# Kernel optimization log

Hardware: AMD Instinct MI355X
Metric: run time of the kernel (lower is better)

## Reference

```python
import jax, jax.numpy as jnp
import numpy as np

N_NODES = 100000
N_EDGES = 1600000
N_DATE = 5000  # last N_DATE nodes are date nodes [0,0,1]
D_IN = 128
D_H = 128
N_CLASSES = 16
MLP_HID = 8


def setup_inputs() -> dict:
    key = jax.random.key(0)
    ks = jax.random.split(key, 12)
    feature = jax.random.normal(ks[0], (N_NODES, D_IN), dtype=jnp.float32)
    edge_weight = jax.random.uniform(ks[1], (N_EDGES,), dtype=jnp.float32)
    src = jax.random.randint(ks[2], (N_EDGES,), 0, N_NODES, dtype=jnp.int32)
    dst = jax.random.randint(ks[3], (N_EDGES,), 0, N_NODES, dtype=jnp.int32)
    # node_type one-hot: regular nodes [1,0,0], last N_DATE nodes are date nodes [0,0,1]
    nt = np.zeros((N_NODES, 3), dtype=np.int32)
    nt[: N_NODES - N_DATE, 0] = 1
    nt[N_NODES - N_DATE :, 2] = 1
    node_type = jnp.asarray(nt)
    # GraphConv weights (xavier uniform) + zero bias, DGL convention: h @ W, W:[in,out]
    def xavier(k, fan_in, fan_out):
        lim = float(np.sqrt(6.0 / (fan_in + fan_out)))
        return jax.random.uniform(k, (fan_in, fan_out), jnp.float32, -lim, lim)
    W0 = xavier(ks[4], D_IN, D_H)
    b0 = jnp.zeros((D_H,), jnp.float32)
    W1 = xavier(ks[5], D_H, D_H)
    b1 = jnp.zeros((D_H,), jnp.float32)
    mlp_w1 = xavier(ks[6], D_H, MLP_HID)
    mlp_b1 = jnp.zeros((MLP_HID,), jnp.float32)
    mlp_w2 = xavier(ks[7], MLP_HID, N_CLASSES)
    mlp_b2 = jnp.zeros((N_CLASSES,), jnp.float32)
    return {
        "feature": feature, "edge_weight": edge_weight, "src": src, "dst": dst,
        "node_type": node_type, "W0": W0, "b0": b0, "W1": W1, "b1": b1,
        "mlp_w1": mlp_w1, "mlp_b1": mlp_b1, "mlp_w2": mlp_w2, "mlp_b2": mlp_b2,
    }


def reference(feature, edge_weight, src, dst, node_type,
              W0, b0, W1, b1, mlp_w1, mlp_b1, mlp_w2, mlp_b2):
    n = feature.shape[0]
    ones_e = jnp.ones_like(edge_weight)
    # unweighted degrees (DGL norm='both'), clamped to >= 1
    deg_out = jnp.clip(jax.ops.segment_sum(ones_e, src, num_segments=n), 1.0)
    deg_in = jnp.clip(jax.ops.segment_sum(ones_e, dst, num_segments=n), 1.0)
    norm_src = deg_out ** -0.5  # [N]
    norm_dst = deg_in ** -0.5   # [N]

    def graph_conv(h, W, b):
        hn = h * norm_src[:, None]                      # D_out^{-1/2} src scaling
        msg = hn[src] * edge_weight[:, None]            # [E, d] edge-weighted gather
        agg = jax.ops.segment_sum(msg, dst, num_segments=n)  # scatter-add
        return (agg * norm_dst[:, None]) @ W + b        # D_in^{-1/2}, then linear

    h = jax.nn.relu(graph_conv(feature, W0, b0))
    h = jax.nn.relu(graph_conv(h, W1, b1))

    # sum-pool over date nodes ([0,0,1]) == tail slice in original layout
    date_mask = ((node_type[:, 0] == 0) & (node_type[:, 1] == 0) & (node_type[:, 2] == 1)).astype(h.dtype)
    cnt = date_mask.sum()
    pooled = (h * date_mask[:, None]).sum(axis=0) / cnt  # [d_h]

    hid = jax.nn.relu(pooled @ mlp_w1 + mlp_b1)
    return hid @ mlp_w2 + mlp_b2  # [num_classes]
```

## Files before the change

kernel.cpp:

```cpp
#include <hip/hip_runtime.h>
#include <hip/hip_fp16.h>
#include <hip/hip_fp8.h>
#include <stdint.h>

#define D 128
#define GT 16
#define SLOTS 48
#define EPB 4096
#define PTB 1024
#define CAPE 5120
#define MAXB 400
#define MAXDATE 8192
#define WPN 16384
#define PWAVES 8

typedef _Float16 f16x8 __attribute__((ext_vector_type(8)));
typedef float    f32x4 __attribute__((ext_vector_type(4)));
typedef float    f32x2 __attribute__((ext_vector_type(2)));

__global__ __launch_bounds__(PTB) void partition_kernel(
    const int* __restrict__ src, const int* __restrict__ dst, const float* __restrict__ ew,
    int* __restrict__ cursorA, int* __restrict__ cursorB,
    int2* __restrict__ ebuf, unsigned char* __restrict__ sbuf, int E, int nbk) {
    __shared__ int histA[MAXB], histB[MAXB], baseA[MAXB], baseB[MAXB];
    int tid = threadIdx.x;
    for (int i = tid; i < nbk; i += PTB) { histA[i] = 0; histB[i] = 0; }
    __syncthreads();
    int e0 = blockIdx.x * EPB;
    int dcache[EPB / PTB], scache[EPB / PTB];
    float wcache[EPB / PTB];
    #pragma unroll
    for (int i = 0; i < EPB / PTB; ++i) {
        int e = e0 + i * PTB + tid;
        bool ok = e < E;
        dcache[i] = ok ? dst[e] : -1;
        scache[i] = ok ? src[e] : 0;
        wcache[i] = ok ? ew[e] : 0.f;
        if (ok) {
            atomicAdd(&histA[dcache[i] >> 8], 1);
            atomicAdd(&histB[scache[i] >> 8], 1);
        }
    }
    __syncthreads();
    for (int i = tid; i < nbk; i += PTB) {
        baseA[i] = atomicAdd(&cursorA[i], histA[i]);
        baseB[i] = atomicAdd(&cursorB[i], histB[i]);
        histA[i] = 0; histB[i] = 0;
    }
    __syncthreads();
    #pragma unroll
    for (int i = 0; i < EPB / PTB; ++i) {
        if (dcache[i] >= 0) {
            int d = dcache[i], s = scache[i];
            int bA = d >> 8;
            int pA = baseA[bA] + atomicAdd(&histA[bA], 1);
            if (pA < CAPE) ebuf[(size_t)bA * CAPE + pA] =
                make_int2(s | ((d & 255) << 17), __float_as_int(wcache[i]));
            int bB = s >> 8;
            int pB = baseB[bB] + atomicAdd(&histB[bB], 1);
            if (pB < CAPE) sbuf[(size_t)bB * CAPE + pB] = (unsigned char)(s & 255);
        }
    }
}

__global__ __launch_bounds__(256) void build_count_kernel(
    const int2* __restrict__ ebuf, const int* __restrict__ cursorA,
    const unsigned char* __restrict__ sbuf, const int* __restrict__ cursorB,
    int2* __restrict__ ell, int* __restrict__ deg_in, int* __restrict__ deg_out,
    int n, int nbk) {
    __shared__ int lcur[256];
    int tid = threadIdx.x;
    lcur[tid] = 0;
    __syncthreads();
    if (blockIdx.x < (unsigned)nbk) {
        int b = blockIdx.x;
        int cntE = min(cursorA[b], CAPE);
        const int2* buf = ebuf + (size_t)b * CAPE;
        for (int i = tid; i < cntE; i += 256) {
            int2 r = buf[i];
            int s = r.x & 0x1FFFF;
            int dlow = (r.x >> 17) & 255;
            int slot = atomicAdd(&lcur[dlow], 1);
            int node = (b << 8) + dlow;
            if (slot < SLOTS) ell[(size_t)node * SLOTS + slot] = make_int2(s, r.y);
        }
        __syncthreads();
        int v = (b << 8) + tid;
        if (v < n) deg_in[v] = lcur[tid];
    } else {
        int b = blockIdx.x - nbk;
        int cntS = min(cursorB[b], CAPE);
        const unsigned char* buf = sbuf + (size_t)b * CAPE;
        const unsigned int* buf32 = (const unsigned int*)buf;
        int nw = cntS >> 2;
        for (int i = tid; i < nw; i += 256) {
            unsigned int wv = buf32[i];
            atomicAdd(&lcur[wv & 255], 1);
            atomicAdd(&lcur[(wv >> 8) & 255], 1);
            atomicAdd(&lcur[(wv >> 16) & 255], 1);
            atomicAdd(&lcur[wv >> 24], 1);
        }
        if (tid < (cntS & 3)) atomicAdd(&lcur[buf[(nw << 2) + tid]], 1);
        __syncthreads();
        int v = (b << 8) + tid;
        if (v < n) deg_out[v] = lcur[tid];
    }
}

__global__ void norm_flag_kernel(const int* __restrict__ deg_out, const int* __restrict__ deg_in,
                                 const int* __restrict__ node_type,
                                 float* __restrict__ norm_src, float* __restrict__ norm_dst,
                                 int* __restrict__ list, int* __restrict__ cnt,
                                 unsigned char* __restrict__ flag, int n) {
    int v = blockIdx.x * blockDim.x + threadIdx.x;
    if (v < n) {
        float d_o = (float)max(deg_out[v], 1);
        float d_i = (float)max(deg_in[v], 1);
        norm_src[v] = 1.0f / sqrtf(d_o);
        norm_dst[v] = 1.0f / sqrtf(d_i);
        flag[v] = 0;
        int t0 = node_type[v * 3 + 0];
        int t1 = node_type[v * 3 + 1];
        int t2 = node_type[v * 3 + 2];
        if (t0 == 0 && t1 == 0 && t2 == 1) {
            int idx = atomicAdd(cnt, 1);
            list[idx] = v;
        }
    }
}

__global__ __launch_bounds__(256) void mark_kernel(
    const int* __restrict__ list, const int* __restrict__ cnt,
    const int2* __restrict__ ell, const int* __restrict__ deg_in,
    unsigned char* __restrict__ flag) {
    int wave = (blockIdx.x * 256 + threadIdx.x) >> 6;
    int lane = threadIdx.x & 63;
    if (wave >= min(*cnt, MAXDATE)) return;
    int v = __builtin_amdgcn_readfirstlane(list[wave]);
    int m = min(deg_in[v], SLOTS);
    if (lane < m) {
        int s = ell[(size_t)v * SLOTS + lane].x;
        flag[s] = 1;
    }
}

__global__ __launch_bounds__(256) void compact_kernel(
    const unsigned char* __restrict__ flag, const int* __restrict__ deg_in,
    int* __restrict__ list2, int* __restrict__ cnt2, int n) {
    int v = blockIdx.x * 256 + threadIdx.x;
    int lane = threadIdx.x & 63;
    bool f = (v < n) && (flag[v] != 0);
    unsigned long long mask = __ballot(f);
    int base = 0;
    if (lane == 0 && mask) base = atomicAdd(cnt2, __popcll(mask));
    base = __shfl(base, 0);
    if (f) {
        int off = __builtin_amdgcn_mbcnt_hi((unsigned int)(mask >> 32),
                  __builtin_amdgcn_mbcnt_lo((unsigned int)mask, 0));
        list2[base + off] = v | (min(deg_in[v], SLOTS) << 17);
    }
}

__global__ __launch_bounds__(256) void wpack_kernel(const float* __restrict__ W,
                                                    _Float16* __restrict__ wp,
                                                    int* __restrict__ cursorAB,
                                                    float* __restrict__ pooled,
                                                    int* __restrict__ cnt) {
    int tid = threadIdx.x;
    if (blockIdx.x == 0) {
        for (int i = tid; i < 2 * MAXB; i += 256) cursorAB[i] = 0;
        if (tid < D) pooled[tid] = 0.f;
        if (tid == 0) { cnt[0] = 0; cnt[1] = 0; }
    }
    int base = blockIdx.x * 256 + tid;
    for (int idx = base; idx < WPN; idx += gridDim.x * 256) {
        int j = idx & 7;
        int l = (idx >> 3) & 63;
        int c = (idx >> 9) & 7;
        int k0b = idx >> 12;
        int q = l >> 4, r = l & 15;
        float w = W[(k0b * 32 + q * 8 + j) * 128 + c * 16 + r];
        _Float16 hi = (_Float16)w;
        wp[idx] = hi;
        wp[idx + WPN] = (_Float16)(w - (float)hi);
    }
}

__global__ __launch_bounds__(512) void gemm_mfma_kernel(
    const float* __restrict__ X, const float* __restrict__ ns,
    const _Float16* __restrict__ wp, unsigned char* __restrict__ P8, int n) {
    __shared__ _Float16 wl[2 * WPN];
    int tid  = threadIdx.x;
    int lane = tid & 63;
    int wib  = tid >> 6;
    {
        const ulonglong2* src16 = (const ulonglong2*)wp;
        ulonglong2* dst16 = (ulonglong2*)wl;
        #pragma unroll
        for (int i = 0; i < (2 * WPN * 2) / (512 * 16); ++i)
            dst16[i * 512 + tid] = src16[i * 512 + tid];
    }
    __syncthreads();

    int q = lane >> 4, r = lane & 15;
    int row0 = blockIdx.x * 128 + wib * 16;
    if (row0 >= n) return;
    int ra = min(row0 + r, n - 1);
    float sa = ns[ra];

    float4 x[8];
    #pragma unroll
    for (int kb = 0; kb < 4; ++kb) {
        x[2 * kb]     = *(const float4*)&X[(size_t)ra * 128 + kb * 32 + q * 8];
        x[2 * kb + 1] = *(const float4*)&X[(size_t)ra * 128 + kb * 32 + q * 8 + 4];
    }
    f16x8 a[4];
    #pragma unroll
    for (int kb = 0; kb < 4; ++kb) {
        a[kb][0] = (_Float16)(x[2 * kb].x * sa);
        a[kb][1] = (_Float16)(x[2 * kb].y * sa);
        a[kb][2] = (_Float16)(x[2 * kb].z * sa);
        a[kb][3] = (_Float16)(x[2 * kb].w * sa);
        a[kb][4] = (_Float16)(x[2 * kb + 1].x * sa);
        a[kb][5] = (_Float16)(x[2 * kb + 1].y * sa);
        a[kb][6] = (_Float16)(x[2 * kb + 1].z * sa);
        a[kb][7] = (_Float16)(x[2 * kb + 1].w * sa);
    }

    f32x4 acc[8];
    #pragma unroll
    for (int c = 0; c < 8; ++c) acc[c] = (f32x4){0.f, 0.f, 0.f, 0.f};

    const _Float16* wb = wl + lane * 8;
    #pragma unroll
    for (int c = 0; c < 8; ++c) {
        #pragma unroll
        for (int kb = 0; kb < 4; ++kb) {
            f16x8 bh = *(const f16x8*)&wb[kb * 4096 + c * 512];
            f16x8 bl = *(const f16x8*)&wb[kb * 4096 + c * 512 + WPN];
            acc[c] = __builtin_amdgcn_mfma_f32_16x16x32_f16(bh, a[kb], acc[c], 0, 0, 0);
            acc[c] = __builtin_amdgcn_mfma_f32_16x16x32_f16(bl, a[kb], acc[c], 0, 0, 0);
        }
    }

    int row = row0 + r;
    if (row < n) {
        #pragma unroll
        for (int c = 0; c < 8; ++c) {
            int w0 = __builtin_amdgcn_cvt_pk_fp8_f32(acc[c][0], acc[c][1], 0, false);
            int w1 = __builtin_amdgcn_cvt_pk_fp8_f32(acc[c][2], acc[c][3], w0, true);
            *(unsigned int*)&P8[(size_t)row * 128 + c * 16 + q * 4] = (unsigned int)w1;
        }
    }
}

__global__ __launch_bounds__(256) void gather1_kernel(
    const unsigned char* __restrict__ P8, const int2* __restrict__ ell,
    const float* __restrict__ norm_src, const float* __restrict__ norm_dst,
    const float* __restrict__ bias, const int* __restrict__ list2,
    const int* __restrict__ cnt2, __half* __restrict__ h1) {
    int wave = (blockIdx.x * 256 + threadIdx.x) >> 6;
    int lane = threadIdx.x & 63;
    int nn = __builtin_amdgcn_readfirstlane(*cnt2);
    if (wave >= nn) return;
    int pk = __builtin_amdgcn_readfirstlane(list2[wave]);
    int v = pk & 0x1FFFF;
    int m = pk >> 17;
    int half = lane >> 5;
    int l32  = lane & 31;
    const int2* row = ell + (size_t)v * SLOTS;
    const unsigned int* P32 = (const unsigned int*)P8;
    float nd = norm_dst[v];
    float ns = norm_src[v];
    float4 acc = make_float4(0.f, 0.f, 0.f, 0.f);

    if (m <= 16) {
        int4 q[8];
        #pragma unroll
        for (int i = 0; i < 8; ++i) q[i] = *(const int4*)&row[2 * i];
        unsigned int r[8];
        float w[8];
        #pragma unroll
        for (int i = 0; i < 8; ++i) {
            bool ok = (2 * i + half) < m;
            int s = ok ? (half ? q[i].z : q[i].x) : 0;
            w[i] = ok ? __int_as_float(half ? q[i].w : q[i].y) : 0.f;
            r[i] = P32[(size_t)s * 32 + l32];
        }
        #pragma unroll
        for (int i = 0; i < 8; ++i) {
            f32x2 c0 = __builtin_amdgcn_cvt_pk_f32_fp8((int)r[i], false);
            f32x2 c1 = __builtin_amdgcn_cvt_pk_f32_fp8((int)r[i], true);
            acc.x = fmaf(w[i], c0[0], acc.x);
            acc.y = fmaf(w[i], c0[1], acc.y);
            acc.z = fmaf(w[i], c1[0], acc.z);
            acc.w = fmaf(w[i], c1[1], acc.w);
        }
    } else {
        int4 q[16];
        #pragma unroll
        for (int i = 0; i < 16; ++i) q[i] = *(const int4*)&row[2 * i];
        unsigned int r[16];
        float w[16];
        #pragma unroll
        for (int i = 0; i < 16; ++i) {
            bool ok = (2 * i + half) < m;
            int s = ok ? (half ? q[i].z : q[i].x) : 0;
            w[i] = ok ? __int_as_float(half ? q[i].w : q[i].y) : 0.f;
            r[i] = P32[(size_t)s * 32 + l32];
        }
        #pragma unroll
        for (int i = 0; i < 16; ++i) {
            f32x2 c0 = __builtin_amdgcn_cvt_pk_f32_fp8((int)r[i], false);
            f32x2 c1 = __builtin_amdgcn_cvt_pk_f32_fp8((int)r[i], true);
            acc.x = fmaf(w[i], c0[0], acc.x);
            acc.y = fmaf(w[i], c0[1], acc.y);
            acc.z = fmaf(w[i], c1[0], acc.z);
            acc.w = fmaf(w[i], c1[1], acc.w);
        }
        if (m > 32) {
            for (int e = 32; e < m; e += 4) {
                int4 qa = *(const int4*)&row[e];
                int4 qb = *(const int4*)&row[e + 2];
                int2 p0 = half ? make_int2(qa.z, qa.w) : make_int2(qa.x, qa.y);
                int2 p1 = half ? make_int2(qb.z, qb.w) : make_int2(qb.x, qb.y);
                bool v0 = (e + half) < m;
                bool v1 = (e + 2 + half) < m;
                int s0 = v0 ? p0.x : 0;
                int s1 = v1 ? p1.x : 0;
                unsigned int r0 = P32[(size_t)s0 * 32 + l32];
                unsigned int r1 = P32[(size_t)s1 * 32 + l32];
                float w0 = v0 ? __int_as_float(p0.y) : 0.f;
                float w1 = v1 ? __int_as_float(p1.y) : 0.f;
                f32x2 c0 = __builtin_amdgcn_cvt_pk_f32_fp8((int)r0, false);
                f32x2 c1 = __builtin_amdgcn_cvt_pk_f32_fp8((int)r0, true);
                f32x2 d0 = __builtin_amdgcn_cvt_pk_f32_fp8((int)r1, false);
                f32x2 d1 = __builtin_amdgcn_cvt_pk_f32_fp8((int)r1, true);
                acc.x = fmaf(w0, c0[0], acc.x); acc.x = fmaf(w1, d0[0], acc.x);
                acc.y = fmaf(w0, c0[1], acc.y); acc.y = fmaf(w1, d0[1], acc.y);
                acc.z = fmaf(w0, c1[0], acc.z); acc.z = fmaf(w1, d1[0], acc.z);
                acc.w = fmaf(w0, c1[1], acc.w); acc.w = fmaf(w1, d1[1], acc.w);
            }
        }
    }

    acc.x += __shfl_xor(acc.x, 32);
    acc.y += __shfl_xor(acc.y, 32);
    acc.z += __shfl_xor(acc.z, 32);
    acc.w += __shfl_xor(acc.w, 32);
    if (half == 0) {
        float4 b4 = ((const float4*)bias)[l32];
        float ra = fmaxf(fmaf(acc.x, nd, b4.x), 0.f) * ns;
        float rb = fmaxf(fmaf(acc.y, nd, b4.y), 0.f) * ns;
        float rc = fmaxf(fmaf(acc.z, nd, b4.z), 0.f) * ns;
        float rd = fmaxf(fmaf(acc.w, nd, b4.w), 0.f) * ns;
        __half2 h0 = __floats2half2_rn(ra, rb);
        __half2 h1v = __floats2half2_rn(rc, rd);
        uint2 u;
        u.x = *(unsigned int*)&h0;
        u.y = *(unsigned int*)&h1v;
        ((uint2*)h1)[(size_t)v * 32 + l32] = u;
    }
}

__global__ __launch_bounds__(256) void gather2_list_kernel(
    const __half* __restrict__ h, const int* __restrict__ deg_in,
    const int2* __restrict__ ell, const float* __restrict__ norm_dst,
    const int* __restrict__ list, const int* __restrict__ cnt,
    float* __restrict__ out) {
    int wave = (blockIdx.x * 256 + threadIdx.x) >> 6;
    int lane = threadIdx.x & 63;
    if (wave >= min(*cnt, MAXDATE)) return;
    int v = __builtin_amdgcn_readfirstlane(list[wave]);
    int half = lane >> 5;
    int l32  = lane & 31;
    const int2* row = ell + (size_t)v * SLOTS;
    int dg = deg_in[v];
    int4 q[16];
    #pragma unroll
    for (int i = 0; i < 16; ++i) q[i] = *(const int4*)&row[2 * i];
    int m = min(dg, SLOTS);
    float2 r[16];
    float w[16];
    #pragma unroll
    for (int i = 0; i < 16; ++i) {
        bool ok = (2 * i + half) < m;
        int s = ok ? (half ? q[i].z : q[i].x) : 0;
        w[i] = ok ? __int_as_float(half ? q[i].w : q[i].y) : 0.f;
        r[i] = ((const float2*)h)[(size_t)s * 32 + l32];
    }
    float4 acc = make_float4(0.f, 0.f, 0.f, 0.f);
    #pragma unroll
    for (int i = 0; i < 16; ++i) {
        float2 a01 = __half22float2(*(const __half2*)&r[i].x);
        float2 a23 = __half22float2(*(const __half2*)&r[i].y);
        acc.x = fmaf(w[i], a01.x, acc.x);
        acc.y = fmaf(w[i], a01.y, acc.y);
        acc.z = fmaf(w[i], a23.x, acc.z);
        acc.w = fmaf(w[i], a23.y, acc.w);
    }
    if (m > 32) {
        for (int e = 32; e < m; e += 4) {
            int4 qa = *(const int4*)&row[e];
            int4 qb = *(const int4*)&row[e + 2];
            int2 p0 = half ? make_int2(qa.z, qa.w) : make_int2(qa.x, qa.y);
            int2 p1 = half ? make_int2(qb.z, qb.w) : make_int2(qb.x, qb.y);
            bool v0 = (e + half) < m;
            bool v1 = (e + 2 + half) < m;
            int s0 = v0 ? p0.x : 0;
            int s1 = v1 ? p1.x : 0;
            float2 raw0 = ((const float2*)h)[(size_t)s0 * 32 + l32];
            float2 raw1 = ((const float2*)h)[(size_t)s1 * 32 + l32];
            float w0 = v0 ? __int_as_float(p0.y) : 0.f;
            float w1 = v1 ? __int_as_float(p1.y) : 0.f;
            float2 a01 = __half22float2(*(const __half2*)&raw0.x);
            float2 a23 = __half22float2(*(const __half2*)&raw0.y);
            float2 b01 = __half22float2(*(const __half2*)&raw1.x);
            float2 b23 = __half22float2(*(const __half2*)&raw1.y);
            acc.x = fmaf(w0, a01.x, acc.x); acc.x = fmaf(w1, b01.x, acc.x);
            acc.y = fmaf(w0, a01.y, acc.y); acc.y = fmaf(w1, b01.y, acc.y);
            acc.z = fmaf(w0, a23.x, acc.z); acc.z = fmaf(w1, b23.x, acc.z);
            acc.w = fmaf(w0, a23.y, acc.w); acc.w = fmaf(w1, b23.y, acc.w);
        }
    }
    acc.x += __shfl_xor(acc.x, 32);
    acc.y += __shfl_xor(acc.y, 32);
    acc.z += __shfl_xor(acc.z, 32);
    acc.w += __shfl_xor(acc.w, 32);
    if (half == 0) {
        float nd = norm_dst[v];
        ((float4*)(out + (size_t)wave * D))[l32] =
            make_float4(acc.x * nd, acc.y * nd, acc.z * nd, acc.w * nd);
    }
}

__global__ __launch_bounds__(512) void gemm_pool_kernel(
    const float* __restrict__ X, const float* __restrict__ W,
    const float* __restrict__ bias, const int* __restrict__ cnt,
    float* __restrict__ pooled) {
    __shared__ float wlds[D * D];
    __shared__ float rows[PWAVES][GT * D];
    int tid  = threadIdx.x;
    int lane = tid & 63;
    int wib  = tid >> 6;

    const float4* W4 = (const float4*)W;
    for (int i = tid; i < (D * D) / 4; i += 512)
        *(float4*)&wlds[i * 4] = W4[i];
    __syncthreads();

    int m = min(*cnt, MAXDATE);
    int ntiles = (m + GT - 1) / GT;
    float2 bb = ((const float2*)bias)[lane];
    float psx = 0.f, psy = 0.f;
    bool any = false;
    float* rw = rows[wib];
    const float2* X2 = (const float2*)X;

    for (int tile = blockIdx.x * PWAVES + wib; tile < ntiles; tile += gridDim.x * PWAVES) {
        int t0 = tile * GT;
        any = true;
        #pragma unroll
        for (int t = 0; t < GT; ++t) {
            int i = t0 + t;
            float2 r = (i < m) ? X2[(size_t)i * 64 + lane] : make_float2(0.f, 0.f);
            *(float2*)&rw[t * D + 2 * lane] = r;
        }
        __builtin_amdgcn_wave_barrier();

        float2 acc[GT];
        #pragma unroll
        for (int t = 0; t < GT; ++t) acc[t] = make_float2(0.f, 0.f);

        for (int k = 0; k < D; k += 4) {
            float2 w0 = *(const float2*)&wlds[(k + 0) * D + 2 * lane];
            float2 w1 = *(const float2*)&wlds[(k + 1) * D + 2 * lane];
            float2 w2 = *(const float2*)&wlds[(k + 2) * D + 2 * lane];
            float2 w3 = *(const float2*)&wlds[(k + 3) * D + 2 * lane];
            #pragma unroll
            for (int t = 0; t < GT; ++t) {
                float4 r = *(const float4*)&rw[t * D + k];
                acc[t].x = fmaf(r.x, w0.x, acc[t].x); acc[t].y = fmaf(r.x, w0.y, acc[t].y);
                acc[t].x = fmaf(r.y, w1.x, acc[t].x); acc[t].y = fmaf(r.y, w1.y, acc[t].y);
                acc[t].x = fmaf(r.z, w2.x, acc[t].x); acc[t].y = fmaf(r.z, w2.y, acc[t].y);
                acc[t].x = fmaf(r.w, w3.x, acc[t].x); acc[t].y = fmaf(r.w, w3.y, acc[t].y);
            }
        }

        #pragma unroll
        for (int t = 0; t < GT; ++t) {
            if (t0 + t < m) {
                psx += fmaxf(acc[t].x + bb.x, 0.f);
                psy += fmaxf(acc[t].y + bb.y, 0.f);
            }
        }
        __builtin_amdgcn_wave_barrier();
    }

    if (any) {
        atomicAdd(&pooled[2 * lane + 0], psx);
        atomicAdd(&pooled[2 * lane + 1], psy);
    }
}

__global__ void mlp_kernel(const float* __restrict__ pooled, const int* __restrict__ cnt,
                           const float* __restrict__ w1, const float* __restrict__ b1,
                           const float* __restrict__ w2, const float* __restrict__ b2,
                           float* __restrict__ out) {
    __shared__ float hid[8];
    int t = threadIdx.x;
    float inv = 1.0f / (float)(*cnt);
    if (t < 8) {
        float a = b1[t];
        for (int k = 0; k < 128; ++k) a = fmaf(pooled[k] * inv, w1[k * 8 + t], a);
        hid[t] = fmaxf(a, 0.f);
    }
    __syncthreads();
    if (t < 16) {
        float a = b2[t];
        for (int j = 0; j < 8; ++j) a = fmaf(hid[j], w2[j * 16 + t], a);
        out[t] = a;
    }
}

extern "C" void kernel_launch(void* const* d_in, const int* in_sizes, int n_in,
                              void* d_out, int out_size, void* d_ws, size_t ws_size,
                              hipStream_t stream) {
    const float* feature   = (const float*)d_in[0];
    const float* ew        = (const float*)d_in[1];
    const int*   src       = (const int*)d_in[2];
    const int*   dst       = (const int*)d_in[3];
    const int*   node_type = (const int*)d_in[4];
    const float* W0        = (const float*)d_in[5];
    const float* b0        = (const float*)d_in[6];
    const float* W1        = (const float*)d_in[7];
    const float* b1        = (const float*)d_in[8];
    const float* mw1       = (const float*)d_in[9];
    const float* mb1       = (const float*)d_in[10];
    const float* mw2       = (const float*)d_in[11];
    const float* mb2       = (const float*)d_in[12];
    float* out = (float*)d_out;

    const int n = in_sizes[0] / D;
    const int E = in_sizes[1];
    const int NBK = (n + 255) >> 8;

    char* ws = (char*)d_ws;
    size_t off = 0;
    auto alloc = [&](size_t bytes) -> void* {
        void* p = ws + off;
        off = (off + bytes + 255) & ~(size_t)255;
        return p;
    };
    int*           cursorAB = (int*)alloc(2 * MAXB * 4);
    int*           deg_in   = (int*)alloc((size_t)n * 4);
    int*           deg_out  = (int*)alloc((size_t)n * 4);
    float*         norm_src = (float*)alloc((size_t)n * 4);
    float*         norm_dst = (float*)alloc((size_t)n * 4);
    int*           list     = (int*)alloc((size_t)n * 4);
    int*           list2    = (int*)alloc((size_t)n * 4);
    unsigned char* flag     = (unsigned char*)alloc((size_t)n);
    int2*          ell      = (int2*)alloc(((size_t)n * SLOTS + 8) * 8);
    int2*          ebuf     = (int2*)alloc((size_t)NBK * CAPE * 8);
    unsigned char* sbuf     = (unsigned char*)alloc((size_t)NBK * CAPE);
    unsigned char* P8       = (unsigned char*)alloc((size_t)n * D);
    __half*        h1       = (__half*)alloc((size_t)n * D * 2);
    _Float16*      wp       = (_Float16*)alloc(2 * WPN * 2);
    float*         pooled   = (float*)alloc(D * 4);
    int*           cnt      = (int*)alloc(256);
    float*         agg      = (float*)ebuf;

    int* cursorA = cursorAB;
    int* cursorB = cursorAB + MAXB;
    int* cnt2    = cnt + 1;

    const int TB = 256;
    int pblk = (E + EPB - 1) / EPB;
    int nblk = (n + TB - 1) / TB;

    wpack_kernel<<<16, TB, 0, stream>>>(W0, wp, cursorAB, pooled, cnt);
    partition_kernel<<<pblk, PTB, 0, stream>>>(src, dst, ew, cursorA, cursorB, ebuf, sbuf, E, NBK);
    build_count_kernel<<<2 * NBK, TB, 0, stream>>>(ebuf, cursorA, sbuf, cursorB,
                                                   ell, deg_in, deg_out, n, NBK);
    norm_flag_kernel<<<nblk, TB, 0, stream>>>(deg_out, deg_in, node_type,
                                              norm_src, norm_dst, list, cnt, flag, n);
    mark_kernel<<<(MAXDATE * 64) / TB, TB, 0, stream>>>(list, cnt, ell, deg_in, flag);
    compact_kernel<<<nblk, TB, 0, stream>>>(flag, deg_in, list2, cnt2, n);

    gemm_mfma_kernel<<<(n + 127) / 128, 512, 0, stream>>>(feature, norm_src, wp, P8, n);

    gather1_kernel<<<(n * 64 + TB - 1) / TB, TB, 0, stream>>>(
        P8, ell, norm_src, norm_dst, b0, list2, cnt2, h1);

    gather2_list_kernel<<<(MAXDATE * 64) / TB, TB, 0, stream>>>(
        h1, deg_in, ell, norm_dst, list, cnt, agg);
    gemm_pool_kernel<<<64, 512, 0, stream>>>(agg, W1, b1, cnt, pooled);

    mlp_kernel<<<1, 64, 0, stream>>>(pooled, cnt, mw1, mb1, mw2, mb2, out);
}
```

Before: 273.3 us.

## Mark date-node sources during partition and fuse norm, flag and compaction kernels

The date-node mask now becomes a bitmap in the weight-pack kernel, which also clears the flag array. The partition kernel marks the source of every edge pointing into a date node directly, so the separate mark kernel that read the ELL rows is gone. Norm computation, date-list building and source compaction are fused into one kernel, cutting two launches and an extra pass over node arrays. The layer-2 gather also gains a short path for nodes with at most 16 in-edges, so fewer unused slot loads are issued. One behaviour change: marking from raw edges counts all in-edges, not only the first SLOTS kept in ELL.

```diff
diff --git a/kernel.cpp b/kernel.cpp
--- a/kernel.cpp
+++ b/kernel.cpp
@@ -18,10 +18,54 @@
 typedef float    f32x4 __attribute__((ext_vector_type(4)));
 typedef float    f32x2 __attribute__((ext_vector_type(2)));
 
+__global__ __launch_bounds__(256) void wpack_kernel(const float* __restrict__ W,
+                                                    _Float16* __restrict__ wp,
+                                                    int* __restrict__ cursorAB,
+                                                    float* __restrict__ pooled,
+                                                    int* __restrict__ cnt,
+                                                    const int* __restrict__ node_type,
+                                                    unsigned int* __restrict__ bitmap,
+                                                    int* __restrict__ flag32, int n) {
+    int tid = threadIdx.x;
+    int gt  = blockIdx.x * 256 + tid;
+    int gsz = gridDim.x * 256;
+    int lane = tid & 63;
+    if (blockIdx.x == 0) {
+        for (int i = tid; i < 2 * MAXB; i += 256) cursorAB[i] = 0;
+        if (tid < D) pooled[tid] = 0.f;
+        if (tid == 0) { cnt[0] = 0; cnt[1] = 0; }
+    }
+    int nround = (n + 63) & ~63;
+    for (int v = gt; v < nround; v += gsz) {
+        bool isd = false;
+        if (v < n) {
+            isd = (node_type[v * 3 + 0] == 0) && (node_type[v * 3 + 1] == 0) &&
+                  (node_type[v * 3 + 2] == 1);
+        }
+        unsigned long long msk = __ballot(isd);
+        if (lane == 0)  bitmap[v >> 5] = (unsigned int)msk;
+        if (lane == 32) bitmap[v >> 5] = (unsigned int)(msk >> 32);
+    }
+    for (int i = gt; i < ((n + 3) >> 2); i += gsz) flag32[i] = 0;
+    for (int idx = gt; idx < WPN; idx += gsz) {
+        int j = idx & 7;
+        int l = (idx >> 3) & 63;
+        int c = (idx >> 9) & 7;
+        int k0b = idx >> 12;
+        int q = l >> 4, r = l & 15;
+        float w = W[(k0b * 32 + q * 8 + j) * 128 + c * 16 + r];
+        _Float16 hi = (_Float16)w;
+        wp[idx] = hi;
+        wp[idx + WPN] = (_Float16)(w - (float)hi);
+    }
+}
+
 __global__ __launch_bounds__(PTB) void partition_kernel(
     const int* __restrict__ src, const int* __restrict__ dst, const float* __restrict__ ew,
     int* __restrict__ cursorA, int* __restrict__ cursorB,
-    int2* __restrict__ ebuf, unsigned char* __restrict__ sbuf, int E, int nbk) {
+    int2* __restrict__ ebuf, unsigned char* __restrict__ sbuf,
+    const unsigned int* __restrict__ bitmap, unsigned char* __restrict__ flag,
+    int E, int nbk) {
     __shared__ int histA[MAXB], histB[MAXB], baseA[MAXB], baseB[MAXB];
     int tid = threadIdx.x;
     for (int i = tid; i < nbk; i += PTB) { histA[i] = 0; histB[i] = 0; }
@@ -29,6 +73,7 @@
     int e0 = blockIdx.x * EPB;
     int dcache[EPB / PTB], scache[EPB / PTB];
     float wcache[EPB / PTB];
+    unsigned int dmask = 0;
     #pragma unroll
     for (int i = 0; i < EPB / PTB; ++i) {
         int e = e0 + i * PTB + tid;
@@ -39,6 +84,7 @@
         if (ok) {
             atomicAdd(&histA[dcache[i] >> 8], 1);
             atomicAdd(&histB[scache[i] >> 8], 1);
+            if ((bitmap[dcache[i] >> 5] >> (dcache[i] & 31)) & 1) dmask |= 1u << i;
         }
     }
     __syncthreads();
@@ -59,6 +105,7 @@
             int bB = s >> 8;
             int pB = baseB[bB] + atomicAdd(&histB[bB], 1);
             if (pB < CAPE) sbuf[(size_t)bB * CAPE + pB] = (unsigned char)(s & 255);
+            if ((dmask >> i) & 1) flag[s] = 1;
         }
     }
 }
@@ -107,49 +154,27 @@
     }
 }
 
-__global__ void norm_flag_kernel(const int* __restrict__ deg_out, const int* __restrict__ deg_in,
-                                 const int* __restrict__ node_type,
-                                 float* __restrict__ norm_src, float* __restrict__ norm_dst,
-                                 int* __restrict__ list, int* __restrict__ cnt,
-                                 unsigned char* __restrict__ flag, int n) {
-    int v = blockIdx.x * blockDim.x + threadIdx.x;
-    if (v < n) {
-        float d_o = (float)max(deg_out[v], 1);
-        float d_i = (float)max(deg_in[v], 1);
-        norm_src[v] = 1.0f / sqrtf(d_o);
-        norm_dst[v] = 1.0f / sqrtf(d_i);
-        flag[v] = 0;
-        int t0 = node_type[v * 3 + 0];
-        int t1 = node_type[v * 3 + 1];
-        int t2 = node_type[v * 3 + 2];
-        if (t0 == 0 && t1 == 0 && t2 == 1) {
-            int idx = atomicAdd(cnt, 1);
-            list[idx] = v;
-        }
-    }
-}
-
-__global__ __launch_bounds__(256) void mark_kernel(
-    const int* __restrict__ list, const int* __restrict__ cnt,
-    const int2* __restrict__ ell, const int* __restrict__ deg_in,
-    unsigned char* __restrict__ flag) {
-    int wave = (blockIdx.x * 256 + threadIdx.x) >> 6;
-    int lane = threadIdx.x & 63;
-    if (wave >= min(*cnt, MAXDATE)) return;
-    int v = __builtin_amdgcn_readfirstlane(list[wave]);
-    int m = min(deg_in[v], SLOTS);
-    if (lane < m) {
-        int s = ell[(size_t)v * SLOTS + lane].x;
-        flag[s] = 1;
-    }
-}
-
-__global__ __launch_bounds__(256) void compact_kernel(
-    const unsigned char* __restrict__ flag, const int* __restrict__ deg_in,
+__global__ __launch_bounds__(256) void norm_compact_kernel(
+    const int* __restrict__ deg_out, const int* __restrict__ deg_in,
+    const unsigned int* __restrict__ bitmap, const unsigned char* __restrict__ flag,
+    float* __restrict__ norm_src, float* __restrict__ norm_dst,
+    int* __restrict__ list, int* __restrict__ cnt,
     int* __restrict__ list2, int* __restrict__ cnt2, int n) {
     int v = blockIdx.x * 256 + threadIdx.x;
     int lane = threadIdx.x & 63;
-    bool f = (v < n) && (flag[v] != 0);
+    bool inb = v < n;
+    int di = 0;
+    if (inb) {
+        int d_o = max(deg_out[v], 1);
+        di = deg_in[v];
+        norm_src[v] = 1.0f / sqrtf((float)d_o);
+        norm_dst[v] = 1.0f / sqrtf((float)max(di, 1));
+        if ((bitmap[v >> 5] >> (v & 31)) & 1) {
+            int idx = atomicAdd(cnt, 1);
+            list[idx] = v;
+        }
+    }
+    bool f = inb && (flag[v] != 0);
     unsigned long long mask = __ballot(f);
     int base = 0;
     if (lane == 0 && mask) base = atomicAdd(cnt2, __popcll(mask));
@@ -157,32 +182,7 @@
     if (f) {
         int off = __builtin_amdgcn_mbcnt_hi((unsigned int)(mask >> 32),
                   __builtin_amdgcn_mbcnt_lo((unsigned int)mask, 0));
-        list2[base + off] = v | (min(deg_in[v], SLOTS) << 17);
-    }
-}
-
-__global__ __launch_bounds__(256) void wpack_kernel(const float* __restrict__ W,
-                                                    _Float16* __restrict__ wp,
-                                                    int* __restrict__ cursorAB,
-                                                    float* __restrict__ pooled,
-                                                    int* __restrict__ cnt) {
-    int tid = threadIdx.x;
-    if (blockIdx.x == 0) {
-        for (int i = tid; i < 2 * MAXB; i += 256) cursorAB[i] = 0;
-        if (tid < D) pooled[tid] = 0.f;
-        if (tid == 0) { cnt[0] = 0; cnt[1] = 0; }
-    }
-    int base = blockIdx.x * 256 + tid;
-    for (int idx = base; idx < WPN; idx += gridDim.x * 256) {
-        int j = idx & 7;
-        int l = (idx >> 3) & 63;
-        int c = (idx >> 9) & 7;
-        int k0b = idx >> 12;
-        int q = l >> 4, r = l & 15;
-        float w = W[(k0b * 32 + q * 8 + j) * 128 + c * 16 + r];
-        _Float16 hi = (_Float16)w;
-        wp[idx] = hi;
-        wp[idx + WPN] = (_Float16)(w - (float)hi);
+        list2[base + off] = v | (min(di, SLOTS) << 17);
     }
 }
 
@@ -375,52 +375,76 @@
     int half = lane >> 5;
     int l32  = lane & 31;
     const int2* row = ell + (size_t)v * SLOTS;
-    int dg = deg_in[v];
-    int4 q[16];
-    #pragma unroll
-    for (int i = 0; i < 16; ++i) q[i] = *(const int4*)&row[2 * i];
-    int m = min(dg, SLOTS);
-    float2 r[16];
-    float w[16];
-    #pragma unroll
-    for (int i = 0; i < 16; ++i) {
-        bool ok = (2 * i + half) < m;
-        int s = ok ? (half ? q[i].z : q[i].x) : 0;
-        w[i] = ok ? __int_as_float(half ? q[i].w : q[i].y) : 0.f;
-        r[i] = ((const float2*)h)[(size_t)s * 32 + l32];
-    }
+    int m = min(__builtin_amdgcn_readfirstlane(deg_in[v]), SLOTS);
     float4 acc = make_float4(0.f, 0.f, 0.f, 0.f);
-    #pragma unroll
-    for (int i = 0; i < 16; ++i) {
-        float2 a01 = __half22float2(*(const __half2*)&r[i].x);
-        float2 a23 = __half22float2(*(const __half2*)&r[i].y);
-        acc.x = fmaf(w[i], a01.x, acc.x);
-        acc.y = fmaf(w[i], a01.y, acc.y);
-        acc.z = fmaf(w[i], a23.x, acc.z);
-        acc.w = fmaf(w[i], a23.y, acc.w);
-    }
-    if (m > 32) {
-        for (int e = 32; e < m; e += 4) {
-            int4 qa = *(const int4*)&row[e];
-            int4 qb = *(const int4*)&row[e + 2];
-            int2 p0 = half ? make_int2(qa.z, qa.w) : make_int2(qa.x, qa.y);
-            int2 p1 = half ? make_int2(qb.z, qb.w) : make_int2(qb.x, qb.y);
-            bool v0 = (e + half) < m;
-            bool v1 = (e + 2 + half) < m;
-            int s0 = v0 ? p0.x : 0;
-            int s1 = v1 ? p1.x : 0;
-            float2 raw0 = ((const float2*)h)[(size_t)s0 * 32 + l32];
-            float2 raw1 = ((const float2*)h)[(size_t)s1 * 32 + l32];
-            float w0 = v0 ? __int_as_float(p0.y) : 0.f;
-            float w1 = v1 ? __int_as_float(p1.y) : 0.f;
-            float2 a01 = __half22float2(*(const __half2*)&raw0.x);
-            float2 a23 = __half22float2(*(const __half2*)&raw0.y);
-            float2 b01 = __half22float2(*(const __half2*)&raw1.x);
-            float2 b23 = __half22float2(*(const __half2*)&raw1.y);
-            acc.x = fmaf(w0, a01.x, acc.x); acc.x = fmaf(w1, b01.x, acc.x);
-            acc.y = fmaf(w0, a01.y, acc.y); acc.y = fmaf(w1, b01.y, acc.y);
-            acc.z = fmaf(w0, a23.x, acc.z); acc.z = fmaf(w1, b23.x, acc.z);
-            acc.w = fmaf(w0, a23.y, acc.w); acc.w = fmaf(w1, b23.y, acc.w);
+
+    if (m <= 16) {
+        int4 q[8];
+        #pragma unroll
+        for (int i = 0; i < 8; ++i) q[i] = *(const int4*)&row[2 * i];
+        float2 r[8];
+        float w[8];
+        #pragma unroll
+        for (int i = 0; i < 8; ++i) {
+            bool ok = (2 * i + half) < m;
+            int s = ok ? (half ? q[i].z : q[i].x) : 0;
+            w[i] = ok ? __int_as_float(half ? q[i].w : q[i].y) : 0.f;
+            r[i] = ((const float2*)h)[(size_t)s * 32 + l32];
+        }
+        #pragma unroll
+        for (int i = 0; i < 8; ++i) {
+            float2 a01 = __half22float2(*(const __half2*)&r[i].x);
+            float2 a23 = __half22float2(*(const __half2*)&r[i].y);
+            acc.x = fmaf(w[i], a01.x, acc.x);
+            acc.y = fmaf(w[i], a01.y, acc.y);
+            acc.z = fmaf(w[i], a23.x, acc.z);
+            acc.w = fmaf(w[i], a23.y, acc.w);
+        }
+    } else {
+        int4 q[16];
+        #pragma unroll
+        for (int i = 0; i < 16; ++i) q[i] = *(const int4*)&row[2 * i];
+        float2 r[16];
+        float w[16];
+        #pragma unroll
+        for (int i = 0; i < 16; ++i) {
+            bool ok = (2 * i + half) < m;
+            int s = ok ? (half ? q[i].z : q[i].x) : 0;
+            w[i] = ok ? __int_as_float(half ? q[i].w : q[i].y) : 0.f;
+            r[i] = ((const float2*)h)[(size_t)s * 32 + l32];
+        }
+        #pragma unroll
+        for (int i = 0; i < 16; ++i) {
+            float2 a01 = __half22float2(*(const __half2*)&r[i].x);
+            float2 a23 = __half22float2(*(const __half2*)&r[i].y);
+            acc.x = fmaf(w[i], a01.x, acc.x);
+            acc.y = fmaf(w[i], a01.y, acc.y);
+            acc.z = fmaf(w[i], a23.x, acc.z);
+            acc.w = fmaf(w[i], a23.y, acc.w);
+        }
+        if (m > 32) {
+            for (int e = 32; e < m; e += 4) {
+                int4 qa = *(const int4*)&row[e];
+                int4 qb = *(const int4*)&row[e + 2];
+                int2 p0 = half ? make_int2(qa.z, qa.w) : make_int2(qa.x, qa.y);
+                int2 p1 = half ? make_int2(qb.z, qb.w) : make_int2(qb.x, qb.y);
+                bool v0 = (e + half) < m;
+                bool v1 = (e + 2 + half) < m;
+                int s0 = v0 ? p0.x : 0;
+                int s1 = v1 ? p1.x : 0;
+                float2 raw0 = ((const float2*)h)[(size_t)s0 * 32 + l32];
+                float2 raw1 = ((const float2*)h)[(size_t)s1 * 32 + l32];
+                float w0 = v0 ? __int_as_float(p0.y) : 0.f;
+                float w1 = v1 ? __int_as_float(p1.y) : 0.f;
+                float2 a01 = __half22float2(*(const __half2*)&raw0.x);
+                float2 a23 = __half22float2(*(const __half2*)&raw0.y);
+                float2 b01 = __half22float2(*(const __half2*)&raw1.x);
+                float2 b23 = __half22float2(*(const __half2*)&raw1.y);
+                acc.x = fmaf(w0, a01.x, acc.x); acc.x = fmaf(w1, b01.x, acc.x);
+                acc.y = fmaf(w0, a01.y, acc.y); acc.y = fmaf(w1, b01.y, acc.y);
+                acc.z = fmaf(w0, a23.x, acc.z); acc.z = fmaf(w1, b23.x, acc.z);
+                acc.w = fmaf(w0, a23.y, acc.w); acc.w = fmaf(w1, b23.y, acc.w);
+            }
         }
     }
     acc.x += __shfl_xor(acc.x, 32);
@@ -559,7 +583,8 @@
     float*         norm_dst = (float*)alloc((size_t)n * 4);
     int*           list     = (int*)alloc((size_t)n * 4);
     int*           list2    = (int*)alloc((size_t)n * 4);
-    unsigned char* flag     = (unsigned char*)alloc((size_t)n);
+    unsigned char* flag     = (unsigned char*)alloc(((size_t)n + 255) & ~(size_t)255);
+    unsigned int*  bitmap   = (unsigned int*)alloc((((size_t)n + 63) / 64 * 2 + 2) * 4);
     int2*          ell      = (int2*)alloc(((size_t)n * SLOTS + 8) * 8);
     int2*          ebuf     = (int2*)alloc((size_t)NBK * CAPE * 8);
     unsigned char* sbuf     = (unsigned char*)alloc((size_t)NBK * CAPE);
@@ -578,14 +603,15 @@
     int pblk = (E + EPB - 1) / EPB;
     int nblk = (n + TB - 1) / TB;
 
-    wpack_kernel<<<16, TB, 0, stream>>>(W0, wp, cursorAB, pooled, cnt);
-    partition_kernel<<<pblk, PTB, 0, stream>>>(src, dst, ew, cursorA, cursorB, ebuf, sbuf, E, NBK);
+    wpack_kernel<<<16, TB, 0, stream>>>(W0, wp, cursorAB, pooled, cnt,
+                                        node_type, bitmap, (int*)flag, n);
+    partition_kernel<<<pblk, PTB, 0, stream>>>(src, dst, ew, cursorA, cursorB,
+                                               ebuf, sbuf, bitmap, flag, E, NBK);
     build_count_kernel<<<2 * NBK, TB, 0, stream>>>(ebuf, cursorA, sbuf, cursorB,
                                                    ell, deg_in, deg_out, n, NBK);
-    norm_flag_kernel<<<nblk, TB, 0, stream>>>(deg_out, deg_in, node_type,
-                                              norm_src, norm_dst, list, cnt, flag, n);
-    mark_kernel<<<(MAXDATE * 64) / TB, TB, 0, stream>>>(list, cnt, ell, deg_in, flag);
-    compact_kernel<<<nblk, TB, 0, stream>>>(flag, deg_in, list2, cnt2, n);
+    norm_compact_kernel<<<nblk, TB, 0, stream>>>(deg_out, deg_in, bitmap, flag,
+                                                 norm_src, norm_dst, list, cnt,
+                                                 list2, cnt2, n);
 
     gemm_mfma_kernel<<<(n + 127) / 128, 512, 0, stream>>>(feature, norm_src, wp, P8, n);
 
```

Result: no change. 278.0 us (+1.7%).
